# Optimization experiments

Hardware: AMD Instinct MI355X
Metric: run time of the kernel (lower is better)

The kernel has to match this reference:

```python
import jax, jax.numpy as jnp
import numpy as np

B, S, K = 256, 50, 8
D, NH, NL = 512, 8, 2
N_KNOWS, N_PROBS = 1000, 20000
L2 = 2 * NL  # forward layers then backward layers, stacked
HD = D // NH
NEG = -1e9


def _ln(x, g, b, eps=1e-5):
    mu = x.mean(-1, keepdims=True)
    v = ((x - mu) ** 2).mean(-1, keepdims=True)
    return (x - mu) * jax.lax.rsqrt(v + eps) * g + b


def _block(x, m, Wq, bq, Wk, bk, Wv, bv, g1, be1, W1, b1, W2, b2, g2, be2):
    # x: [3B,S,D], m: [3B,1,S,S] additive-OR mask (True = blocked)
    Bx, Sx, Dx = x.shape
    Q = (x @ Wq + bq).reshape(Bx, Sx, NH, HD)
    Kt = (x @ Wk + bk).reshape(Bx, Sx, NH, HD)
    V = (x @ Wv + bv).reshape(Bx, Sx, NH, HD)
    a = jnp.einsum('bqnh,bknh->bnqk', Q, Kt) * (HD ** -0.5)
    a = jnp.where(m, NEG, a)
    p = jax.nn.softmax(a, axis=-1)
    p = jnp.where(m, 0.0, p)  # masked_fill + softmax + where, as in torch source
    o = jnp.einsum('bnqk,bknh->bqnh', p, V).reshape(Bx, Sx, Dx)
    x = _ln(x + o, g1, be1)
    h = jnp.maximum(x @ W1 + b1, 0.0) @ W2 + b2
    return _ln(x + h, g2, be2)


def _forward(probs_his, knows_his, corrs_his, knows_tab, probs_tab, types_tab, pos_tab,
             Wq, bq, Wk, bk, Wv, bv, g1, be1, W1, b1, W2, b2, g2, be2,
             pW1, pb1, pW2, pb2, pW3, pb3):
    info = knows_tab[knows_his].sum(-2) + probs_tab[probs_his] + pos_tab[jnp.arange(S)][None]
    c = corrs_his
    right_t = jnp.where(c, 1, 2)   # corrs==False -> 2
    wrong_t = jnp.where(c, 2, 0)   # corrs==True  -> 2
    norm_t = c.astype(jnp.int32)
    # fold the 3 counterfactual passes (right / wrong / normal) into the batch dim
    x3 = jnp.concatenate([info + types_tab[right_t], info + types_tab[wrong_t], info + types_tab[norm_t]], 0)
    kpm = jnp.tile(probs_his == 0, (3, 1))               # key padding mask [3B,S]
    km = kpm[:, :, None] | kpm[:, None, :]               # OR-combined [3B,S,S]
    tri = jnp.triu(jnp.ones((S, S), bool), 1)
    fm = (tri[None] | km)[:, None]                       # forward (causal) mask
    bm = (tri.T[None] | km)[:, None]                     # backward (anti-causal) mask
    f = x3
    b = x3
    for i in range(NL):
        f = _block(f, fm, Wq[i], bq[i], Wk[i], bk[i], Wv[i], bv[i], g1[i], be1[i], W1[i], b1[i], W2[i], b2[i], g2[i], be2[i])
    for i in range(NL, L2):
        b = _block(b, bm, Wq[i], bq[i], Wk[i], bk[i], Wv[i], bv[i], g1[i], be1[i], W1[i], b1[i], W2[i], b2[i], g2[i], be2[i])
    out = jnp.concatenate([b[:, :1], f[:, :-2] + b[:, 2:], f[:, -1:]], 1)
    h = jnp.concatenate([out, jnp.tile(info, (3, 1, 1))], -1)
    h = jnp.maximum(h @ pW1 + pb1, 0.0)
    h = jnp.maximum(h @ pW2 + pb2, 0.0)
    sc = jax.nn.sigmoid((h @ pW3 + pb3)[..., 0]).reshape(3, B, S)
    # zero out padded positions instead of ragged boolean gather (fixed shape, jit-safe)
    return jnp.where((probs_his > 0)[None], sc, 0.0)


def setup_inputs() -> dict:
    key = jax.random.key(0)
    ks = jax.random.split(key, 16)
    sc = 0.02
    d = {}
    d['probs_his'] = jax.random.randint(ks[0], (B, S), 0, N_PROBS)
    d['knows_his'] = jax.random.randint(ks[1], (B, S, K), 0, N_KNOWS + 1)
    d['corrs_his'] = jax.random.randint(ks[2], (B, S), 0, 2).astype(bool)
    d['knows_tab'] = (jax.random.normal(ks[3], (N_KNOWS + 1, D)) * sc).at[0].set(0.0)  # padding_idx=0
    d['probs_tab'] = (jax.random.normal(ks[4], (N_PROBS + 1, D)) * sc).at[0].set(0.0)
    d['types_tab'] = jax.random.normal(ks[5], (3, D)) * sc
    d['pos_tab'] = jax.random.normal(ks[6], (50, D)) * sc
    d['Wq'] = jax.random.normal(ks[7], (L2, D, D)) * sc
    d['Wk'] = jax.random.normal(ks[8], (L2, D, D)) * sc
    d['Wv'] = jax.random.normal(ks[9], (L2, D, D)) * sc
    d['W1'] = jax.random.normal(ks[10], (L2, D, D)) * sc
    d['W2'] = jax.random.normal(ks[11], (L2, D, D)) * sc
    for n in ('bq', 'bk', 'bv', 'b1', 'b2', 'be1', 'be2'):
        d[n] = jnp.zeros((L2, D))
    d['g1'] = jnp.ones((L2, D))
    d['g2'] = jnp.ones((L2, D))
    d['pW1'] = jax.random.normal(ks[12], (2 * D, D)) * sc
    d['pb1'] = jnp.zeros((D,))
    d['pW2'] = jax.random.normal(ks[13], (D, D // 2)) * sc
    d['pb2'] = jnp.zeros((D // 2,))
    d['pW3'] = jax.random.normal(ks[14], (D // 2, 1)) * sc
    d['pb3'] = jnp.zeros((1,))
    return d


def reference(probs_his, knows_his, corrs_his, knows_tab, probs_tab, types_tab, pos_tab,
              Wq, bq, Wk, bk, Wv, bv, g1, be1, W1, b1, W2, b2, g2, be2,
              pW1, pb1, pW2, pb2, pW3, pb3):
    return _forward(probs_his, knows_his, corrs_his, knows_tab, probs_tab, types_tab, pos_tab,
                    Wq, bq, Wk, bk, Wv, bv, g1, be1, W1, b1, W2, b2, g2, be2,
                    pW1, pb1, pW2, pb2, pW3, pb3)
```

## Files before the change

kernel.cpp:

```cpp
#include <hip/hip_runtime.h>
#include <hip/hip_bf16.h>

#define SEQ 50
#define DD  512
#define NHD 8
#define HDIM 64
#define MPROWS 38400
#define MTROWS 76800

typedef __hip_bfloat16 bf;
typedef __attribute__((ext_vector_type(8))) short bf16x8;
typedef __attribute__((ext_vector_type(4))) float f32x4;

__device__ __forceinline__ float bf2f(unsigned short u) {
    unsigned int x = ((unsigned int)u) << 16;
    return __builtin_bit_cast(float, x);
}
__device__ __forceinline__ unsigned short f2bu(float f) {
    unsigned int u = __builtin_bit_cast(unsigned int, f);
    u += 0x7fffu + ((u >> 16) & 1u);
    return (unsigned short)(u >> 16);
}

#define ASYNC16(g, l) __builtin_amdgcn_global_load_lds( \
    (__attribute__((address_space(1))) void*)(g),       \
    (__attribute__((address_space(3))) void*)(l), 16, 0, 0)

__global__ __launch_bounds__(256) void transpose_cast(
    const float* __restrict__ src, bf* __restrict__ dst,
    int R, int C, size_t sStride, size_t dStride)
{
    __shared__ float tile[32][33];
    int l = blockIdx.z;
    src += (size_t)l * sStride;
    dst += (size_t)l * dStride;
    int c0 = blockIdx.x * 32, r0 = blockIdx.y * 32;
    int tx = threadIdx.x & 31, ty = threadIdx.x >> 5;
    for (int i = ty; i < 32; i += 8)
        tile[i][tx] = src[(size_t)(r0 + i) * C + c0 + tx];
    __syncthreads();
    for (int i = ty; i < 32; i += 8)
        dst[(size_t)(c0 + i) * R + r0 + tx] = __float2bfloat16(tile[tx][i]);
}

__global__ __launch_bounds__(256) void biascat_kernel(
    const float* __restrict__ bq, const float* __restrict__ bk,
    const float* __restrict__ bv, float* __restrict__ out)
{
    int i = blockIdx.x * 256 + threadIdx.x;
    if (i >= 4 * 1536) return;
    int l = i / 1536, c = i % 1536;
    float v;
    if (c < 512)       v = bq[l * 512 + c];
    else if (c < 1024) v = bk[l * 512 + c - 512];
    else               v = bv[l * 512 + c - 1024];
    out[i] = v;
}

__global__ __launch_bounds__(256) void tproj_kernel(
    const float* __restrict__ types_tab, const bf* __restrict__ WTqkv,
    bf* __restrict__ Tt)
{
    int gid = blockIdx.x * 256 + threadIdx.x;
    if (gid >= 9216) return;
    int hl = gid / 4608;
    int t  = (gid / 1536) % 3;
    int n  = gid % 1536;
    const unsigned short* w =
        (const unsigned short*)(WTqkv + (size_t)(hl * 2) * 786432 + (size_t)n * 512);
    const float* ty = types_tab + t * 512;
    float a = 0.f;
    for (int k = 0; k < 512; ++k) a += ty[k] * bf2f(w[k]);
    Tt[gid] = __float2bfloat16(a);
}

__global__ __launch_bounds__(256) void embed_kernel(
    const int* __restrict__ probs_his, const int* __restrict__ knows_his,
    const int* __restrict__ corrs, const float* __restrict__ knows_tab,
    const float* __restrict__ probs_tab, const float* __restrict__ types_tab,
    const float* __restrict__ pos_tab, bf* __restrict__ info, bf* __restrict__ X)
{
    int bs = blockIdx.x * 4 + (threadIdx.x >> 6);
    int lane = threadIdx.x & 63;
    int s = bs % SEQ;
    int p = probs_his[bs];
    int c = corrs[bs];
    int d0 = lane * 8;

    float v[8];
    #pragma unroll
    for (int j = 0; j < 8; ++j)
        v[j] = probs_tab[(size_t)p * DD + d0 + j] + pos_tab[(size_t)s * DD + d0 + j];
    for (int k = 0; k < 8; ++k) {
        int ki = knows_his[bs * 8 + k];
        const float* kr = knows_tab + (size_t)ki * DD + d0;
        #pragma unroll
        for (int j = 0; j < 8; ++j) v[j] += kr[j];
    }
    int t0 = c ? 1 : 2;
    int t1 = c ? 2 : 0;
    int t2 = c ? 1 : 0;
    const float* T0 = types_tab + t0 * DD + d0;
    const float* T1 = types_tab + t1 * DD + d0;
    const float* T2 = types_tab + t2 * DD + d0;
    uint4 xi, x0, x1, x2;
    unsigned short* pi = (unsigned short*)&xi;
    unsigned short* p0 = (unsigned short*)&x0;
    unsigned short* p1 = (unsigned short*)&x1;
    unsigned short* p2 = (unsigned short*)&x2;
    #pragma unroll
    for (int j = 0; j < 8; ++j) {
        pi[j] = f2bu(v[j]);
        p0[j] = f2bu(v[j] + T0[j]);
        p1[j] = f2bu(v[j] + T1[j]);
        p2[j] = f2bu(v[j] + T2[j]);
    }
    size_t base = (size_t)bs * DD + d0;
    const size_t PB = (size_t)12800 * DD;
    *(uint4*)(info + base) = xi;
    *(uint4*)(X + 0 * PB + base) = x0;
    *(uint4*)(X + 1 * PB + base) = x1;
    *(uint4*)(X + 2 * PB + base) = x2;
    *(uint4*)(X + 3 * PB + base) = x0;
    *(uint4*)(X + 4 * PB + base) = x1;
    *(uint4*)(X + 5 * PB + base) = x2;
}

template <int RELU>
__global__ __launch_bounds__(256) void gemm_bt(
    const bf* __restrict__ Ap, const bf* __restrict__ WT0, const bf* __restrict__ WT1,
    const float* __restrict__ bias0, const float* __restrict__ bias1,
    bf* __restrict__ Cp, int N, int Kd, int nN, int mtHalf)
{
    __shared__ bf Al[128 * 64];
    __shared__ bf Bl[128 * 64];
    int nwg = gridDim.x;
    int f = blockIdx.x;
    int q8 = nwg >> 3, r8 = nwg & 7;
    int xcd = f & 7, pos = f >> 3;
    int e = (xcd < r8 ? xcd * (q8 + 1) : r8 * (q8 + 1) + (xcd - r8) * q8) + pos;
    int bm = e / nN, bn = e - bm * nN;
    const bf* WTp;
    const float* bias;
    if (bm < mtHalf) { WTp = WT0; bias = bias0; }
    else             { WTp = WT1; bias = bias1; }
    int m0 = bm * 128, n0 = bn * 128;
    int t = threadIdx.x, lane = t & 63, wave = t >> 6;
    int wr = wave >> 1, wc = wave & 1;
    int lr = lane & 15, lg = lane >> 4;

    f32x4 acc[4][4];
    #pragma unroll
    for (int m = 0; m < 4; ++m)
        #pragma unroll
        for (int n = 0; n < 4; ++n)
            acc[m][n] = (f32x4){0.f, 0.f, 0.f, 0.f};

    for (int kt = 0; kt < Kd; kt += 64) {
        #pragma unroll
        for (int i = 0; i < 4; ++i) {
            int c = i * 256 + t;
            int row = c >> 3, col = (c & 7) * 8;
            ASYNC16(Ap  + (size_t)(m0 + row) * Kd + kt + col, Al + c * 8);
            ASYNC16(WTp + (size_t)(n0 + row) * Kd + kt + col, Bl + c * 8);
        }
        __syncthreads();
        #pragma unroll
        for (int kk = 0; kk < 64; kk += 32) {
            int ko = kk + lg * 8;
            bf16x8 af[4], bfr[4];
            #pragma unroll
            for (int m = 0; m < 4; ++m)
                af[m] = *(const bf16x8*)(Al + (wr * 64 + m * 16 + lr) * 64 + ko);
            #pragma unroll
            for (int n = 0; n < 4; ++n)
                bfr[n] = *(const bf16x8*)(Bl + (wc * 64 + n * 16 + lr) * 64 + ko);
            #pragma unroll
            for (int m = 0; m < 4; ++m)
                #pragma unroll
                for (int n = 0; n < 4; ++n)
                    acc[m][n] = __builtin_amdgcn_mfma_f32_16x16x32_bf16(af[m], bfr[n], acc[m][n], 0, 0, 0);
        }
        __syncthreads();
    }
    unsigned short* Cs = (unsigned short*)Cp;
    #pragma unroll
    for (int n = 0; n < 4; ++n) {
        int col = n0 + wc * 64 + n * 16 + lr;
        float bvv = bias[col];
        #pragma unroll
        for (int m = 0; m < 4; ++m) {
            #pragma unroll
            for (int r = 0; r < 4; ++r) {
                int row = m0 + wr * 64 + m * 16 + lg * 4 + r;
                float v = acc[m][n][r] + bvv;
                if (RELU) v = fmaxf(v, 0.f);
                Cs[(size_t)row * N + col] = f2bu(v);
            }
        }
    }
}

template <int RELU>
__global__ __launch_bounds__(512, 2) void gemm8(
    const bf* __restrict__ Ap, const bf* __restrict__ WT0, const bf* __restrict__ WT1,
    const float* __restrict__ bias0, const float* __restrict__ bias1,
    bf* __restrict__ Cp, int N, int Kd, int nN, int mtHalf)
{
    __shared__ __align__(16) bf As[2][16384];
    __shared__ __align__(16) bf Bs[2][16384];

    int nwg = gridDim.x, f = blockIdx.x;
    int q8 = nwg >> 3, r8 = nwg & 7;
    int xcd = f & 7, pos = f >> 3;
    int e = (xcd < r8 ? xcd * (q8 + 1) : r8 * (q8 + 1) + (xcd - r8) * q8) + pos;
    int bm = e / nN, bn = e - bm * nN;
    const bf* WTp;
    const float* bias;
    if (bm < mtHalf) { WTp = WT0; bias = bias0; }
    else             { WTp = WT1; bias = bias1; }
    int m0 = bm * 256, n0 = bn * 256;
    int t = threadIdx.x, lane = t & 63, wave = t >> 6;
    int wm = wave >> 2, wn = wave & 3;
    int lr = lane & 15, kg = lane >> 4;

    int srow = t >> 3;
    int scolb = (t & 7) * 16;
    const bf* Abase = Ap + (size_t)m0 * Kd;
    const bf* Bbase = WTp + (size_t)n0 * Kd;

#define STG(dsts, base, half, kt) do {                                        \
    _Pragma("unroll")                                                         \
    for (int _i = 0; _i < 2; ++_i) {                                          \
        int _r = (half) * 128 + _i * 64 + srow;                               \
        ASYNC16((base) + (size_t)_r * Kd + (kt) +                             \
                    ((scolb ^ ((_r & 7) << 4)) >> 1),                         \
                (dsts) + _r * 64 + (t & 7) * 8);                              \
    } } while (0)

    f32x4 acc[8][4];
    #pragma unroll
    for (int m = 0; m < 8; ++m)
        #pragma unroll
        for (int n = 0; n < 4; ++n)
            acc[m][n] = (f32x4){0.f, 0.f, 0.f, 0.f};

    STG(As[0], Abase, 0, 0);
    STG(As[0], Abase, 1, 0);
    STG(Bs[0], Bbase, 0, 0);
    STG(Bs[0], Bbase, 1, 0);

    int ntile = Kd >> 6;
    bf16x8 breg[4][2];
    for (int j = 0; j < ntile; ++j) {
        int d = j & 1;
        const char* Ab = (const char*)As[d];
        const char* Bb = (const char*)Bs[d];
        asm volatile("s_waitcnt vmcnt(0)" ::: "memory");
        __builtin_amdgcn_s_barrier();
        int kt1 = (j + 1) << 6;
        int pf = (j + 1 < ntile);
        #pragma unroll
        for (int q = 0; q < 4; ++q) {
            if (q == 0) {
                #pragma unroll
                for (int ns = 0; ns < 4; ++ns) {
                    int row = wn * 64 + ns * 16 + lr;
                    int sw = (row & 7) << 4;
                    breg[ns][0] = *(const bf16x8*)(Bb + row * 128 + ((kg * 16) ^ sw));
                    breg[ns][1] = *(const bf16x8*)(Bb + row * 128 + ((64 + kg * 16) ^ sw));
                }
            }
            bf16x8 areg[2][2];
            #pragma unroll
            for (int mm = 0; mm < 2; ++mm) {
                int row = wm * 128 + (2 * q + mm) * 16 + lr;
                int sw = (row & 7) << 4;
                areg[mm][0] = *(const bf16x8*)(Ab + row * 128 + ((kg * 16) ^ sw));
                areg[mm][1] = *(const bf16x8*)(Ab + row * 128 + ((64 + kg * 16) ^ sw));
            }
            if (pf) {
                if (q == 0)      STG(As[d ^ 1], Abase, 0, kt1);
                else if (q == 1) STG(As[d ^ 1], Abase, 1, kt1);
                else if (q == 2) STG(Bs[d ^ 1], Bbase, 0, kt1);
                else             STG(Bs[d ^ 1], Bbase, 1, kt1);
            }
            __builtin_amdgcn_s_barrier();
            __builtin_amdgcn_s_setprio(1);
            #pragma unroll
            for (int mm = 0; mm < 2; ++mm)
                #pragma unroll
                for (int ns = 0; ns < 4; ++ns) {
                    acc[2 * q + mm][ns] = __builtin_amdgcn_mfma_f32_16x16x32_bf16(
                        areg[mm][0], breg[ns][0], acc[2 * q + mm][ns], 0, 0, 0);
                    acc[2 * q + mm][ns] = __builtin_amdgcn_mfma_f32_16x16x32_bf16(
                        areg[mm][1], breg[ns][1], acc[2 * q + mm][ns], 0, 0, 0);
                }
            __builtin_amdgcn_s_setprio(0);
            if (q != 3) __builtin_amdgcn_s_barrier();
        }
    }
#undef STG

    __syncthreads();
    {
        char* base = (wm == 0) ? (char*)&As[0][0] : (char*)&Bs[0][0];
        #pragma unroll
        for (int ns = 0; ns < 4; ++ns) {
            int col = wn * 64 + ns * 16 + lr;
            float bvv = bias[n0 + col];
            #pragma unroll
            for (int ms = 0; ms < 8; ++ms) {
                #pragma unroll
                for (int rr = 0; rr < 4; ++rr) {
                    int r128 = ms * 16 + kg * 4 + rr;
                    float v = acc[ms][ns][rr] + bvv;
                    if (RELU) v = fmaxf(v, 0.f);
                    *(unsigned short*)(base + r128 * 512 +
                        ((col * 2) ^ ((r128 & 7) << 4))) = f2bu(v);
                }
            }
        }
    }
    __syncthreads();
    {
        unsigned short* Cs = (unsigned short*)Cp;
        int row = t >> 1, hb = (t & 1) * 256;
        int r128 = row & 127;
        const char* src = (row < 128) ? (const char*)&As[0][0] : (const char*)&Bs[0][0];
        char* Crow = (char*)(Cs + (size_t)(m0 + row) * N + n0);
        int sw = (r128 & 7) << 4;
        #pragma unroll
        for (int i2 = 0; i2 < 16; ++i2) {
            int cb = hb + i2 * 16;
            uint4 v = *(const uint4*)(src + r128 * 512 + (cb ^ sw));
            *(uint4*)(Crow + cb) = v;
        }
    }
}

__global__ __launch_bounds__(256) void gemm_head(
    const bf* __restrict__ Ap, const bf* __restrict__ WTp,
    const bf* __restrict__ IPp, bf* __restrict__ Cp, int nN)
{
    __shared__ bf Al[128 * 64];
    __shared__ bf Bl[128 * 64];
    const int Kd = 512, N = 512;
    int nwg = gridDim.x;
    int f = blockIdx.x;
    int q8 = nwg >> 3, r8 = nwg & 7;
    int xcd = f & 7, pos = f >> 3;
    int e = (xcd < r8 ? xcd * (q8 + 1) : r8 * (q8 + 1) + (xcd - r8) * q8) + pos;
    int bm = e / nN, bn = e - bm * nN;
    int m0 = bm * 128, n0 = bn * 128;
    int t = threadIdx.x, lane = t & 63, wave = t >> 6;
    int wr = wave >> 1, wc = wave & 1;
    int lr = lane & 15, lg = lane >> 4;

    f32x4 acc[4][4];
    #pragma unroll
    for (int m = 0; m < 4; ++m)
        #pragma unroll
        for (int n = 0; n < 4; ++n)
            acc[m][n] = (f32x4){0.f, 0.f, 0.f, 0.f};

    for (int kt = 0; kt < Kd; kt += 64) {
        #pragma unroll
        for (int i = 0; i < 4; ++i) {
            int c = i * 256 + t;
            int row = c >> 3, col = (c & 7) * 8;
            ASYNC16(Ap  + (size_t)(m0 + row) * Kd + kt + col, Al + c * 8);
            ASYNC16(WTp + (size_t)(n0 + row) * Kd + kt + col, Bl + c * 8);
        }
        __syncthreads();
        #pragma unroll
        for (int kk = 0; kk < 64; kk += 32) {
            int ko = kk + lg * 8;
            bf16x8 af[4], bfr[4];
            #pragma unroll
            for (int m = 0; m < 4; ++m)
                af[m] = *(const bf16x8*)(Al + (wr * 64 + m * 16 + lr) * 64 + ko);
            #pragma unroll
            for (int n = 0; n < 4; ++n)
                bfr[n] = *(const bf16x8*)(Bl + (wc * 64 + n * 16 + lr) * 64 + ko);
            #pragma unroll
            for (int m = 0; m < 4; ++m)
                #pragma unroll
                for (int n = 0; n < 4; ++n)
                    acc[m][n] = __builtin_amdgcn_mfma_f32_16x16x32_bf16(af[m], bfr[n], acc[m][n], 0, 0, 0);
        }
        __syncthreads();
    }
    unsigned short* Cs = (unsigned short*)Cp;
    const unsigned short* IPu = (const unsigned short*)IPp;
    #pragma unroll
    for (int n = 0; n < 4; ++n) {
        int col = n0 + wc * 64 + n * 16 + lr;
        #pragma unroll
        for (int m = 0; m < 4; ++m) {
            #pragma unroll
            for (int r = 0; r < 4; ++r) {
                int row = m0 + wr * 64 + m * 16 + lg * 4 + r;
                int rr = row % 12800;
                float v = acc[m][n][r] + bf2f(IPu[(size_t)rr * 512 + col]);
                v = fmaxf(v, 0.f);
                Cs[(size_t)row * N + col] = f2bu(v);
            }
        }
    }
}

template <int L0>
__global__ __launch_bounds__(128, 2) void attn_mfma(
    const bf* __restrict__ QKVc, const int* __restrict__ probs_his,
    bf* __restrict__ Oc, int seq0,
    const bf* __restrict__ Tsel, const int* __restrict__ corrs)
{
    __shared__ bf Pl_s[2][4096];
    __shared__ bf Vt_s[2][4096];
    int wave = threadIdx.x >> 6, lane = threadIdx.x & 63;
    bf* Pl = Pl_s[wave];
    bf* Vt = Vt_s[wave];
    int task = blockIdx.x * 2 + wave;
    int h = task & 7, seqL = task >> 3;
    int seqG = seq0 + seqL;
    int st = seqG / 768, b = seqG % 256;
    int pass = (seqG % 768) / 256;
    int lr = lane & 15, kg = lane >> 4;
    size_t qkrow = L0 ? (size_t)b * SEQ : (size_t)seqL * SEQ;
    const bf* Qb = QKVc + qkrow * 1536 + h * HDIM;
    const bf* Kb = Qb + 512;
    const bf* Vb = Qb + 1024;
    const unsigned short* Tu = (const unsigned short*)Tsel;

    int pvv = (lane < SEQ) ? probs_his[b * SEQ + lane] : 1;
    unsigned long long padm = __ballot(pvv == 0) | 0xFFFC000000000000ull;

    #pragma unroll
    for (int it = 0; it < 8; ++it) {
        int idx = it * 64 + lane;
        int key = idx >> 3, d0 = (idx & 7) * 8;
        uint4 v4 = make_uint4(0u, 0u, 0u, 0u);
        if (key < SEQ) v4 = *(const uint4*)(Vb + (size_t)key * 1536 + d0);
        unsigned short* vs = (unsigned short*)&v4;
        if (L0) {
            int kk2 = (key < SEQ) ? key : (SEQ - 1);
            int cc = corrs[b * SEQ + kk2];
            int tt = (pass == 0) ? (cc ? 1 : 2) : (pass == 1) ? (cc ? 2 : 0) : (cc ? 1 : 0);
            const unsigned short* Tv = Tu + tt * 1536 + 1024 + h * HDIM + d0;
            #pragma unroll
            for (int j = 0; j < 8; ++j)
                vs[j] = f2bu(bf2f(vs[j]) + bf2f(Tv[j]));
        }
        #pragma unroll
        for (int j = 0; j < 8; ++j) {
            int d = d0 + j;
            int byt = (d * 128 + key * 2) ^ ((j & 7) << 4);
            *(unsigned short*)((char*)Vt + byt) = vs[j];
        }
    }

    bf16x8 kf[4][2], qf[4][2];
    #pragma unroll
    for (int m = 0; m < 4; ++m) {
        int rk = 16 * m + lr; if (rk > SEQ - 1) rk = SEQ - 1;
        int tt = 0;
        if (L0) {
            int cc = corrs[b * SEQ + rk];
            tt = (pass == 0) ? (cc ? 1 : 2) : (pass == 1) ? (cc ? 2 : 0) : (cc ? 1 : 0);
        }
        #pragma unroll
        for (int kb = 0; kb < 2; ++kb) {
            kf[m][kb] = *(const bf16x8*)(Kb + (size_t)rk * 1536 + kb * 32 + kg * 8);
            qf[m][kb] = *(const bf16x8*)(Qb + (size_t)rk * 1536 + kb * 32 + kg * 8);
            if (L0) {
                const unsigned short* Tq = Tu + tt * 1536 + h * HDIM + kb * 32 + kg * 8;
                #pragma unroll
                for (int j = 0; j < 8; ++j) {
                    qf[m][kb][j] = (short)f2bu(bf2f((unsigned short)qf[m][kb][j]) + bf2f(Tq[j]));
                    kf[m][kb][j] = (short)f2bu(bf2f((unsigned short)kf[m][kb][j]) + bf2f(Tq[512 + j]));
                }
            }
        }
    }
    f32x4 sacc[4][4];
    #pragma unroll
    for (int m = 0; m < 4; ++m)
        #pragma unroll
        for (int n = 0; n < 4; ++n)
            sacc[m][n] = (f32x4){0.f, 0.f, 0.f, 0.f};
    #pragma unroll
    for (int kb = 0; kb < 2; ++kb)
        #pragma unroll
        for (int m = 0; m < 4; ++m)
            #pragma unroll
            for (int n = 0; n < 4; ++n)
                sacc[m][n] = __builtin_amdgcn_mfma_f32_16x16x32_bf16(kf[m][kb], qf[n][kb], sacc[m][n], 0, 0, 0);

    #pragma unroll
    for (int n = 0; n < 4; ++n) {
        int q = 16 * n + lr;
        int qpad = (int)((padm >> q) & 1ull);
        float p[4][4];
        float mx = -3e38f;
        #pragma unroll
        for (int m = 0; m < 4; ++m)
            #pragma unroll
            for (int r = 0; r < 4; ++r) {
                int key = 16 * m + 4 * kg + r;
                int blocked = qpad | (int)((padm >> key) & 1ull) |
                              (st == 0 ? (key > q) : (key < q));
                float s = sacc[m][n][r] * 0.125f;
                p[m][r] = blocked ? -3e38f : s;
                if (!blocked) mx = fmaxf(mx, s);
            }
        mx = fmaxf(mx, __shfl_xor(mx, 16));
        mx = fmaxf(mx, __shfl_xor(mx, 32));
        float sum = 0.f;
        #pragma unroll
        for (int m = 0; m < 4; ++m)
            #pragma unroll
            for (int r = 0; r < 4; ++r) {
                float e = (p[m][r] > -1e37f) ? __expf(p[m][r] - mx) : 0.f;
                p[m][r] = e;
                sum += e;
            }
        sum += __shfl_xor(sum, 16);
        sum += __shfl_xor(sum, 32);
        float inv = (sum > 0.f) ? 1.f / sum : 0.f;
        #pragma unroll
        for (int m = 0; m < 4; ++m) {
            unsigned int u0 = (unsigned int)f2bu(p[m][0] * inv) |
                              ((unsigned int)f2bu(p[m][1] * inv) << 16);
            unsigned int u1 = (unsigned int)f2bu(p[m][2] * inv) |
                              ((unsigned int)f2bu(p[m][3] * inv) << 16);
            int base = (q * 128 + (16 * m + 4 * kg) * 2) ^ ((q & 7) << 4);
            *(unsigned int*)((char*)Pl + base) = u0;
            *(unsigned int*)((char*)Pl + base + 4) = u1;
        }
    }

    f32x4 oacc[4][4];
    #pragma unroll
    for (int m = 0; m < 4; ++m)
        #pragma unroll
        for (int n = 0; n < 4; ++n)
            oacc[m][n] = (f32x4){0.f, 0.f, 0.f, 0.f};
    #pragma unroll
    for (int kb = 0; kb < 2; ++kb) {
        bf16x8 vf[4], pf[4];
        #pragma unroll
        for (int m = 0; m < 4; ++m) {
            int row = 16 * m + lr;
            int byt = (row * 128 + (kb * 32 + kg * 8) * 2) ^ ((row & 7) << 4);
            vf[m] = *(const bf16x8*)((char*)Vt + byt);
            pf[m] = *(const bf16x8*)((char*)Pl + byt);
        }
        #pragma unroll
        for (int m = 0; m < 4; ++m)
            #pragma unroll
            for (int n = 0; n < 4; ++n)
                oacc[m][n] = __builtin_amdgcn_mfma_f32_16x16x32_bf16(vf[m], pf[n], oacc[m][n], 0, 0, 0);
    }
    #pragma unroll
    for (int n = 0; n < 4; ++n) {
        int q = 16 * n + lr;
        if (q < SEQ) {
            #pragma unroll
            for (int m = 0; m < 4; ++m) {
                uint2 ov;
                ov.x = (unsigned int)f2bu(oacc[m][n][0]) | ((unsigned int)f2bu(oacc[m][n][1]) << 16);
                ov.y = (unsigned int)f2bu(oacc[m][n][2]) | ((unsigned int)f2bu(oacc[m][n][3]) << 16);
                *(uint2*)(Oc + (size_t)(seqL * SEQ + q) * DD + h * HDIM + 16 * m + 4 * kg) = ov;
            }
        }
    }
}

__global__ __launch_bounds__(256) void ln_kernel(
    bf* __restrict__ X, const bf* __restrict__ Rb,
    const float* __restrict__ g_all, const float* __restrict__ be_all,
    int lf, int lb)
{
    int row = blockIdx.x * 4 + (threadIdx.x >> 6);
    int lane = threadIdx.x & 63;
    int layer = (row < MPROWS) ? lf : lb;
    const float* g = g_all + layer * DD;
    const float* be = be_all + layer * DD;
    uint4 xa = *((const uint4*)(X + (size_t)row * DD) + lane);
    uint4 ra = *((const uint4*)(Rb + (size_t)row * DD) + lane);
    unsigned short* xs = (unsigned short*)&xa;
    unsigned short* rs = (unsigned short*)&ra;
    float v[8];
    float sum = 0.f;
    #pragma unroll
    for (int j = 0; j < 8; ++j) { v[j] = bf2f(xs[j]) + bf2f(rs[j]); sum += v[j]; }
    #pragma unroll
    for (int o = 1; o < 64; o <<= 1) sum += __shfl_xor(sum, o);
    float mu = sum * (1.f / 512.f);
    float ss = 0.f;
    #pragma unroll
    for (int j = 0; j < 8; ++j) { float d = v[j] - mu; ss += d * d; }
    #pragma unroll
    for (int o = 1; o < 64; o <<= 1) ss += __shfl_xor(ss, o);
    float inv = rsqrtf(ss * (1.f / 512.f) + 1e-5f);
    int d0 = lane * 8;
    uint4 ov;
    unsigned short* os = (unsigned short*)&ov;
    #pragma unroll
    for (int j = 0; j < 8; ++j)
        os[j] = f2bu((v[j] - mu) * inv * g[d0 + j] + be[d0 + j]);
    *((uint4*)(X + (size_t)row * DD) + lane) = ov;
}

__global__ __launch_bounds__(256) void combine_kernel(
    const bf* __restrict__ X, const bf* __restrict__ info,
    bf* __restrict__ Hinc, int rh0, int hstride, int withInfo)
{
    int rl = blockIdx.x * 4 + (threadIdx.x >> 6);
    int rh = rh0 + rl;
    int lane = threadIdx.x & 63;
    int s = rh % SEQ, pb = rh / SEQ, b = pb & 255;
    const size_t MPD = (size_t)MPROWS * DD;
    uint4 o;
    if (s == 0) {
        o = *((const uint4*)(X + MPD + (size_t)(pb * SEQ) * DD) + lane);
    } else if (s == SEQ - 1) {
        o = *((const uint4*)(X + (size_t)(pb * SEQ + SEQ - 1) * DD) + lane);
    } else {
        uint4 a = *((const uint4*)(X + (size_t)(pb * SEQ + s - 1) * DD) + lane);
        uint4 c2 = *((const uint4*)(X + MPD + (size_t)(pb * SEQ + s + 1) * DD) + lane);
        unsigned short* as = (unsigned short*)&a;
        unsigned short* cs = (unsigned short*)&c2;
        unsigned short* os = (unsigned short*)&o;
        #pragma unroll
        for (int j = 0; j < 8; ++j) os[j] = f2bu(bf2f(as[j]) + bf2f(cs[j]));
    }
    *((uint4*)(Hinc + (size_t)rl * hstride) + lane) = o;
    if (withInfo) {
        uint4 iv = *((const uint4*)(info + (size_t)(b * SEQ + s) * DD) + lane);
        *((uint4*)(Hinc + (size_t)rl * hstride + 512) + lane) = iv;
    }
}

__global__ __launch_bounds__(256) void head_final(
    const bf* __restrict__ h2c, const float* __restrict__ pW3,
    const float* __restrict__ pb3, const int* __restrict__ probs_his,
    float* __restrict__ out, int rh0)
{
    int rl = blockIdx.x * 4 + (threadIdx.x >> 6);
    int row = rh0 + rl;
    int lane = threadIdx.x & 63;
    uint2 hv = *((const uint2*)(h2c + (size_t)rl * 256) + lane);
    unsigned short* hs = (unsigned short*)&hv;
    float s = 0.f;
    #pragma unroll
    for (int j = 0; j < 4; ++j) s += bf2f(hs[j]) * pW3[lane * 4 + j];
    #pragma unroll
    for (int o = 1; o < 64; o <<= 1) s += __shfl_xor(s, o);
    if (lane == 0) {
        float logit = s + pb3[0];
        float sc = 1.f / (1.f + __expf(-logit));
        int bb = (row / SEQ) & 255, ss2 = row % SEQ;
        out[row] = (probs_his[bb * SEQ + ss2] > 0) ? sc : 0.f;
    }
}

extern "C" void kernel_launch(void* const* d_in, const int* in_sizes, int n_in,
                              void* d_out, int out_size, void* d_ws, size_t ws_size,
                              hipStream_t stream) {
    const int*   probs_his = (const int*)d_in[0];
    const int*   knows_his = (const int*)d_in[1];
    const int*   corrs     = (const int*)d_in[2];
    const float* knows_tab = (const float*)d_in[3];
    const float* probs_tab = (const float*)d_in[4];
    const float* types_tab = (const float*)d_in[5];
    const float* pos_tab   = (const float*)d_in[6];
    const float* Wq = (const float*)d_in[7];
    const float* Wk = (const float*)d_in[8];
    const float* Wv = (const float*)d_in[9];
    const float* W1 = (const float*)d_in[10];
    const float* W2 = (const float*)d_in[11];
    const float* bq = (const float*)d_in[12];
    const float* bk = (const float*)d_in[13];
    const float* bv = (const float*)d_in[14];
    const float* b1 = (const float*)d_in[15];
    const float* b2 = (const float*)d_in[16];
    const float* be1 = (const float*)d_in[17];
    const float* be2 = (const float*)d_in[18];
    const float* g1 = (const float*)d_in[19];
    const float* g2 = (const float*)d_in[20];
    const float* pW1 = (const float*)d_in[21];
    const float* pb1 = (const float*)d_in[22];
    const float* pW2 = (const float*)d_in[23];
    const float* pb2 = (const float*)d_in[24];
    const float* pW3 = (const float*)d_in[25];
    const float* pb3 = (const float*)d_in[26];

    char* ws = (char*)d_ws;
    bf* WTqkv = (bf*)(ws + 0);
    bf* WT1   = (bf*)(ws + 6291456);
    bf* WT2   = (bf*)(ws + 8388608);
    bf* pW1T  = (bf*)(ws + 10485760);
    bf* pW1aT = (bf*)(ws + 11534336);
    bf* pW1bT = (bf*)(ws + 12058624);
    bf* pW2T  = (bf*)(ws + 12582912);
    float* bqkv = (float*)(ws + 12845056);
    bf* info  = (bf*)(ws + 12869632);
    bf* X     = (bf*)(ws + 25976832);
    const size_t FIXED = 104620032ull;
    const size_t FULLSCR = (size_t)38400 * 4096;

    int CR;
    if      (ws_size >= FIXED + FULLSCR)                  CR = 38400;
    else if (ws_size >= FIXED + (size_t)19200 * 4096)     CR = 19200;
    else if (ws_size >= FIXED + (size_t)9600  * 4096)     CR = 9600;
    else                                                  CR = 3200;
    const int full = (CR == 38400) &&
        (ws_size >= FIXED + FULLSCR + 18432);
    bf* Tt = (bf*)(ws + FIXED + FULLSCR);

    char* SCR = ws + FIXED;

    biascat_kernel<<<dim3(24), dim3(256), 0, stream>>>(bq, bk, bv, bqkv);
    transpose_cast<<<dim3(16,16,4), dim3(256), 0, stream>>>(Wq, WTqkv,          512, 512, 262144, 786432);
    transpose_cast<<<dim3(16,16,4), dim3(256), 0, stream>>>(Wk, WTqkv + 262144, 512, 512, 262144, 786432);
    transpose_cast<<<dim3(16,16,4), dim3(256), 0, stream>>>(Wv, WTqkv + 524288, 512, 512, 262144, 786432);
    transpose_cast<<<dim3(16,16,4), dim3(256), 0, stream>>>(W1, WT1, 512, 512, 262144, 262144);
    transpose_cast<<<dim3(16,16,4), dim3(256), 0, stream>>>(W2, WT2, 512, 512, 262144, 262144);
    transpose_cast<<<dim3(16,32,1), dim3(256), 0, stream>>>(pW1, pW1T, 1024, 512, 0, 0);
    transpose_cast<<<dim3(16,16,1), dim3(256), 0, stream>>>(pW1, pW1aT, 512, 512, 0, 0);
    transpose_cast<<<dim3(16,16,1), dim3(256), 0, stream>>>(pW1 + 262144, pW1bT, 512, 512, 0, 0);
    transpose_cast<<<dim3(8,16,1),  dim3(256), 0, stream>>>(pW2, pW2T, 512, 256, 0, 0);
    embed_kernel<<<dim3(3200), dim3(256), 0, stream>>>(probs_his, knows_his, corrs,
        knows_tab, probs_tab, types_tab, pos_tab, info, X);
    if (full)
        tproj_kernel<<<dim3(36), dim3(256), 0, stream>>>(types_tab, WTqkv, Tt);

    const int BIG = 1 << 30;

    if (full) {
        bf* QKVc = (bf*)SCR;
        bf* Oc   = (bf*)(SCR + (size_t)38400 * 3072);
        bf* F1c  = (bf*)SCR;
        bf* F2c  = (bf*)(SCR + (size_t)76800 * 1024);
        bf* Hin  = (bf*)SCR;
        bf* h1c  = (bf*)(SCR + 39321600);
        bf* h2c  = (bf*)(SCR + 78643200);
        bf* IPb  = (bf*)(SCR + 98304000);

        for (int i = 0; i < 2; ++i) {
            for (int hlf = 0; hlf < 2; ++hlf) {
                int lidx = i + 2 * hlf;
                bf* Xh = X + (size_t)hlf * 38400 * DD;
                const bf* WTq = WTqkv + (size_t)lidx * 786432;
                if (i == 0) {
                    gemm8<0><<<dim3(300), dim3(512), 0, stream>>>(
                        info, WTq, WTq, bqkv + lidx * 1536, bqkv + lidx * 1536,
                        QKVc, 1536, 512, 6, BIG);
                    attn_mfma<1><<<dim3(3072), dim3(128), 0, stream>>>(
                        QKVc, probs_his, Oc, hlf * 768, Tt + hlf * 4608, corrs);
                } else {
                    gemm8<0><<<dim3(900), dim3(512), 0, stream>>>(
                        Xh, WTq, WTq, bqkv + lidx * 1536, bqkv + lidx * 1536,
                        QKVc, 1536, 512, 6, BIG);
                    attn_mfma<0><<<dim3(3072), dim3(128), 0, stream>>>(
                        QKVc, probs_his, Oc, hlf * 768, nullptr, nullptr);
                }
                ln_kernel<<<dim3(9600), dim3(256), 0, stream>>>(
                    Xh, Oc, g1, be1, lidx, lidx);
            }
            gemm8<1><<<dim3(600), dim3(512), 0, stream>>>(
                X, WT1 + (size_t)i * 262144, WT1 + (size_t)(i + 2) * 262144,
                b1 + i * 512, b1 + (i + 2) * 512, F1c, 512, 512, 2, 150);
            gemm8<0><<<dim3(600), dim3(512), 0, stream>>>(
                F1c, WT2 + (size_t)i * 262144, WT2 + (size_t)(i + 2) * 262144,
                b2 + i * 512, b2 + (i + 2) * 512, F2c, 512, 512, 2, 150);
            ln_kernel<<<dim3(19200), dim3(256), 0, stream>>>(
                X, F2c, g2, be2, i, i + 2);
        }

        combine_kernel<<<dim3(9600), dim3(256), 0, stream>>>(X, info, Hin, 0, 512, 0);
        gemm_bt<0><<<dim3(400), dim3(256), 0, stream>>>(
            info, pW1bT, pW1bT, pb1, pb1, IPb, 512, 512, 4, BIG);
        gemm_head<<<dim3(1200), dim3(256), 0, stream>>>(Hin, pW1aT, IPb, h1c, 4);
        gemm_bt<1><<<dim3(600), dim3(256), 0, stream>>>(
            h1c, pW2T, pW2T, pb2, pb2, h2c, 256, 512, 2, BIG);
        head_final<<<dim3(9600), dim3(256), 0, stream>>>(
            h2c, pW3, pb3, probs_his, (float*)d_out, 0);
        return;
    }

    bf* QKVc = (bf*)SCR;
    bf* Oc   = (bf*)(SCR + (size_t)CR * 3072);
    bf* F1c  = (bf*)SCR;
    bf* F2c  = (bf*)(SCR + (size_t)CR * 1024);
    bf* Hinc = (bf*)SCR;
    bf* h1c  = (bf*)(SCR + (size_t)CR * 2048);
    bf* h2c  = (bf*)(SCR + (size_t)CR * 3072);

    const int nck = 38400 / CR;
    const int MT = CR / 128;
    for (int i = 0; i < 2; ++i) {
        for (int hlf = 0; hlf < 2; ++hlf) {
            int lidx = i + 2 * hlf;
            const bf* WTq  = WTqkv + (size_t)lidx * 786432;
            const bf* WT1l = WT1   + (size_t)lidx * 262144;
            const bf* WT2l = WT2   + (size_t)lidx * 262144;
            for (int c = 0; c < nck; ++c) {
                int r0 = hlf * 38400 + c * CR;
                gemm_bt<0><<<dim3(MT * 12), dim3(256), 0, stream>>>(
                    X + (size_t)r0 * DD, WTq, WTq, bqkv + lidx * 1536,
                    bqkv + lidx * 1536, QKVc, 1536, 512, 12, BIG);
                attn_mfma<0><<<dim3((CR/50) * 4), dim3(128), 0, stream>>>(
                    QKVc, probs_his, Oc, r0 / 50, nullptr, nullptr);
                ln_kernel<<<dim3(CR/4), dim3(256), 0, stream>>>(
                    X + (size_t)r0 * DD, Oc, g1, be1, lidx, lidx);
            }
            for (int c = 0; c < nck; ++c) {
                int r0 = hlf * 38400 + c * CR;
                gemm_bt<1><<<dim3(MT * 4), dim3(256), 0, stream>>>(
                    X + (size_t)r0 * DD, WT1l, WT1l, b1 + lidx * 512,
                    b1 + lidx * 512, F1c, 512, 512, 4, BIG);
                gemm_bt<0><<<dim3(MT * 4), dim3(256), 0, stream>>>(
                    F1c, WT2l, WT2l, b2 + lidx * 512, b2 + lidx * 512,
                    F2c, 512, 512, 4, BIG);
                ln_kernel<<<dim3(CR/4), dim3(256), 0, stream>>>(
                    X + (size_t)r0 * DD, F2c, g2, be2, lidx, lidx);
            }
        }
    }
    for (int c = 0; c < nck; ++c) {
        int rh0 = c * CR;
        combine_kernel<<<dim3(CR/4), dim3(256), 0, stream>>>(X, info, Hinc, rh0, 1024, 1);
        gemm_bt<1><<<dim3(MT * 4), dim3(256), 0, stream>>>(
            Hinc, pW1T, pW1T, pb1, pb1, h1c, 512, 1024, 4, BIG);
        gemm_bt<1><<<dim3(MT * 2), dim3(256), 0, stream>>>(
            h1c, pW2T, pW2T, pb2, pb2, h2c, 256, 512, 2, BIG);
        head_final<<<dim3(CR/4), dim3(256), 0, stream>>>(
            h2c, pW3, pb3, probs_his, (float*)d_out, rh0);
    }
}
```

Baseline: 1.183 ms.

## Simplify gemm8 epilogue and route FFN GEMMs to 128-tile gemm_bt kernel

The 256x256 gemm8 loses its dual-weight selection and its LDS-staged coalesced epilogue, so it now writes bf16 results straight from registers to global memory. The two FFN GEMMs, which pick weights per row half, move from gemm8 with 600 blocks to gemm_bt with 128x128 tiles and 2400 blocks. This trades per-block reuse for more parallelism and less LDS pressure. Direct scattered 2-byte stores in gemm8 may coalesce worse than the removed staged writes.

```diff
diff --git a/kernel.cpp b/kernel.cpp
--- a/kernel.cpp
+++ b/kernel.cpp
@@ -203,9 +203,9 @@
 
 template <int RELU>
 __global__ __launch_bounds__(512, 2) void gemm8(
-    const bf* __restrict__ Ap, const bf* __restrict__ WT0, const bf* __restrict__ WT1,
-    const float* __restrict__ bias0, const float* __restrict__ bias1,
-    bf* __restrict__ Cp, int N, int Kd, int nN, int mtHalf)
+    const bf* __restrict__ Ap, const bf* __restrict__ WTp,
+    const float* __restrict__ bias, bf* __restrict__ Cp,
+    int N, int Kd, int nN)
 {
     __shared__ __align__(16) bf As[2][16384];
     __shared__ __align__(16) bf Bs[2][16384];
@@ -215,10 +215,6 @@
     int xcd = f & 7, pos = f >> 3;
     int e = (xcd < r8 ? xcd * (q8 + 1) : r8 * (q8 + 1) + (xcd - r8) * q8) + pos;
     int bm = e / nN, bn = e - bm * nN;
-    const bf* WTp;
-    const float* bias;
-    if (bm < mtHalf) { WTp = WT0; bias = bias0; }
-    else             { WTp = WT1; bias = bias1; }
     int m0 = bm * 256, n0 = bn * 256;
     int t = threadIdx.x, lane = t & 63, wave = t >> 6;
     int wm = wave >> 2, wn = wave & 3;
@@ -302,39 +298,20 @@
     }
 #undef STG
 
-    __syncthreads();
-    {
-        char* base = (wm == 0) ? (char*)&As[0][0] : (char*)&Bs[0][0];
-        #pragma unroll
-        for (int ns = 0; ns < 4; ++ns) {
-            int col = wn * 64 + ns * 16 + lr;
-            float bvv = bias[n0 + col];
-            #pragma unroll
-            for (int ms = 0; ms < 8; ++ms) {
-                #pragma unroll
-                for (int rr = 0; rr < 4; ++rr) {
-                    int r128 = ms * 16 + kg * 4 + rr;
-                    float v = acc[ms][ns][rr] + bvv;
-                    if (RELU) v = fmaxf(v, 0.f);
-                    *(unsigned short*)(base + r128 * 512 +
-                        ((col * 2) ^ ((r128 & 7) << 4))) = f2bu(v);
-                }
-            }
-        }
-    }
-    __syncthreads();
-    {
-        unsigned short* Cs = (unsigned short*)Cp;
-        int row = t >> 1, hb = (t & 1) * 256;
-        int r128 = row & 127;
-        const char* src = (row < 128) ? (const char*)&As[0][0] : (const char*)&Bs[0][0];
-        char* Crow = (char*)(Cs + (size_t)(m0 + row) * N + n0);
-        int sw = (r128 & 7) << 4;
-        #pragma unroll
-        for (int i2 = 0; i2 < 16; ++i2) {
-            int cb = hb + i2 * 16;
-            uint4 v = *(const uint4*)(src + r128 * 512 + (cb ^ sw));
-            *(uint4*)(Crow + cb) = v;
+    unsigned short* Cs = (unsigned short*)Cp;
+    #pragma unroll
+    for (int ns = 0; ns < 4; ++ns) {
+        int col = n0 + wn * 64 + ns * 16 + lr;
+        float bvv = bias[col];
+        #pragma unroll
+        for (int ms = 0; ms < 8; ++ms) {
+            #pragma unroll
+            for (int rr = 0; rr < 4; ++rr) {
+                int row = m0 + wm * 128 + ms * 16 + kg * 4 + rr;
+                float v = acc[ms][ns][rr] + bvv;
+                if (RELU) v = fmaxf(v, 0.f);
+                Cs[(size_t)row * N + col] = f2bu(v);
+            }
         }
     }
 }
@@ -756,26 +733,24 @@
                 const bf* WTq = WTqkv + (size_t)lidx * 786432;
                 if (i == 0) {
                     gemm8<0><<<dim3(300), dim3(512), 0, stream>>>(
-                        info, WTq, WTq, bqkv + lidx * 1536, bqkv + lidx * 1536,
-                        QKVc, 1536, 512, 6, BIG);
+                        info, WTq, bqkv + lidx * 1536, QKVc, 1536, 512, 6);
                     attn_mfma<1><<<dim3(3072), dim3(128), 0, stream>>>(
                         QKVc, probs_his, Oc, hlf * 768, Tt + hlf * 4608, corrs);
                 } else {
                     gemm8<0><<<dim3(900), dim3(512), 0, stream>>>(
-                        Xh, WTq, WTq, bqkv + lidx * 1536, bqkv + lidx * 1536,
-                        QKVc, 1536, 512, 6, BIG);
+                        Xh, WTq, bqkv + lidx * 1536, QKVc, 1536, 512, 6);
                     attn_mfma<0><<<dim3(3072), dim3(128), 0, stream>>>(
                         QKVc, probs_his, Oc, hlf * 768, nullptr, nullptr);
                 }
                 ln_kernel<<<dim3(9600), dim3(256), 0, stream>>>(
                     Xh, Oc, g1, be1, lidx, lidx);
             }
-            gemm8<1><<<dim3(600), dim3(512), 0, stream>>>(
+            gemm_bt<1><<<dim3(2400), dim3(256), 0, stream>>>(
                 X, WT1 + (size_t)i * 262144, WT1 + (size_t)(i + 2) * 262144,
-                b1 + i * 512, b1 + (i + 2) * 512, F1c, 512, 512, 2, 150);
-            gemm8<0><<<dim3(600), dim3(512), 0, stream>>>(
+                b1 + i * 512, b1 + (i + 2) * 512, F1c, 512, 512, 4, 300);
+            gemm_bt<0><<<dim3(2400), dim3(256), 0, stream>>>(
                 F1c, WT2 + (size_t)i * 262144, WT2 + (size_t)(i + 2) * 262144,
-                b2 + i * 512, b2 + (i + 2) * 512, F2c, 512, 512, 2, 150);
+                b2 + i * 512, b2 + (i + 2) * 512, F2c, 512, 512, 4, 300);
             ln_kernel<<<dim3(19200), dim3(256), 0, stream>>>(
                 X, F2c, g2, be2, i, i + 2);
         }
```

Result: faster. 1.090 ms, median of 2 (-7.9%).
